# Kernel tuning notes

Measured on AMD Instinct MI355X. Metric: run time of the kernel, lower is better.

## Reference

```python
import jax, jax.numpy as jnp
import numpy as np

BLANK = 0


def setup_inputs() -> dict:
    key = jax.random.key(0)
    k1, k2 = jax.random.split(key)
    B, T, V = 64, 4096, 128
    feature = jax.random.normal(k1, (B, T, V), dtype=jnp.float32)
    lengths = jax.random.randint(k2, (B,), 1, T + 1, dtype=jnp.int32)
    return {"feature": feature, "lengths": lengths, "beam_width": 1}


def reference(feature, lengths, beam_width):
    # Greedy CTC decode (beam_width <= 1 path of the torch module), fully vectorized.
    # feature: (B, T, V) raw logits; lengths: (B,) valid frame counts.
    B, T, V = feature.shape
    logp = jax.nn.log_softmax(feature.astype(jnp.float32), axis=-1)  # (B, T, V)
    max_scores = jnp.max(logp, axis=-1)                               # (B, T)
    tokens = jnp.argmax(logp, axis=-1).astype(jnp.int32)              # (B, T)

    tmask = jnp.arange(T)[None, :] < lengths[:, None]                 # (B, T) valid frames
    logp_scores = jnp.sum(jnp.where(tmask, max_scores, 0.0), axis=-1) # (B,)

    # CTC collapse: keep token iff it is not blank and differs from previous frame's token.
    # (t != prev or prev == blank) and t != blank  ==  (t != blank) and (t != prev)
    prev = jnp.concatenate(
        [jnp.full((B, 1), BLANK, dtype=tokens.dtype), tokens[:, :-1]], axis=1
    )
    keep = (tokens != BLANK) & (tokens != prev) & tmask               # (B, T)

    # Fixed-shape encoding of the ragged prediction lists:
    # tokens[b, t] is part of prediction[b] (in time order) wherever keep[b, t].
    return tokens, keep, logp_scores
```

## Files before the change

kernel.cpp:

```cpp
#include <hip/hip_runtime.h>

#define BLANK 0

__global__ __launch_bounds__(256) void ctc_rowmax(const float* __restrict__ feat,
                                                  float* __restrict__ out_tok,
                                                  float* __restrict__ row_score,
                                                  int BT)
{
    int pair = blockIdx.x * 4 + (threadIdx.x >> 6);
    int lane = threadIdx.x & 63;
    int l32  = lane & 31;
    int row  = pair * 2 + (lane >> 5);
    if (row >= BT) return;

    const float4* p = (const float4*)(feat + (size_t)pair * 256);
    float4 v = p[lane];

    float m = v.x; int idx = l32 * 4;
    if (v.y > m) { m = v.y; idx = l32 * 4 + 1; }
    if (v.z > m) { m = v.z; idx = l32 * 4 + 2; }
    if (v.w > m) { m = v.w; idx = l32 * 4 + 3; }

    #pragma unroll
    for (int off = 16; off >= 1; off >>= 1) {
        float om = __shfl_xor(m, off, 64);
        int   oi = __shfl_xor(idx, off, 64);
        if (om > m || (om == m && oi < idx)) { m = om; idx = oi; }
    }

    float s = __expf(v.x - m) + __expf(v.y - m) + __expf(v.z - m) + __expf(v.w - m);
    #pragma unroll
    for (int off = 16; off >= 1; off >>= 1) s += __shfl_xor(s, off, 64);

    if (l32 == 0) {
        out_tok[row]   = (float)idx;
        row_score[row] = -__logf(s);
    }
}

__global__ __launch_bounds__(256) void ctc_collapse(const int* __restrict__ lengths,
                                                    const float* __restrict__ out_tok,
                                                    float* __restrict__ keepbuf,
                                                    float* __restrict__ scores,
                                                    int T)
{
    int b = blockIdx.y;
    int t = blockIdx.x * 256 + threadIdx.x;
    float contrib = 0.0f;
    if (t < T) {
        int len = lengths[b];
        size_t base = (size_t)b * T;
        int tk   = (int)out_tok[base + t];
        int prev = (t == 0) ? BLANK : (int)out_tok[base + t - 1];
        float sc = keepbuf[base + t];
        bool valid = t < len;
        keepbuf[base + t] = (tk != BLANK && tk != prev && valid) ? 1.0f : 0.0f;
        contrib = valid ? sc : 0.0f;
    }
    #pragma unroll
    for (int off = 32; off >= 1; off >>= 1) contrib += __shfl_xor(contrib, off, 64);
    if ((threadIdx.x & 63) == 0) atomicAdd(&scores[b], contrib);
}

extern "C" void kernel_launch(void* const* d_in, const int* in_sizes, int n_in,
                              void* d_out, int out_size, void* d_ws, size_t ws_size,
                              hipStream_t stream) {
    const float* feat    = (const float*)d_in[0];
    const int*   lengths = (const int*)d_in[1];

    const int V  = 128;
    const int B  = in_sizes[1];
    const int T  = in_sizes[0] / (B * V);
    const int BT = B * T;

    float* out_tok  = (float*)d_out;
    float* keepbuf  = (float*)d_out + (size_t)BT;
    float* scores   = (float*)d_out + (size_t)2 * BT;

    int pairs  = (BT + 1) / 2;
    int blocks = (pairs + 3) / 4;
    ctc_rowmax<<<blocks, 256, 0, stream>>>(feat, out_tok, keepbuf, BT);

    hipMemsetAsync((void*)scores, 0, (size_t)B * sizeof(float), stream);

    dim3 grid2((T + 255) / 256, B);
    ctc_collapse<<<grid2, 256, 0, stream>>>(lengths, out_tok, keepbuf, scores, T);
}
```

Before: 216.7 us.

## Fuse masked score reduction into rowmax with grid-stride loop and per-8-row partials

The rowmax kernel becomes a grid-stride loop over groups of 8 rows per wavefront with four float4 loads in flight. It computes the log-softmax max as m - log(sum exp(x)) without max subtraction, picks the argmax via ballot instead of index shuffles, and applies the length mask in-kernel, writing one partial sum per 8 rows to workspace. The collapse kernel drops the per-row score buffer read, the memset and the atomics, reducing partials in block 0 of each batch row. Risks: unshifted expf can overflow for large logits, and the shift/mask indexing assumes T is a power of two and BT divisible by 8.

```diff
diff --git a/kernel.cpp b/kernel.cpp
--- a/kernel.cpp
+++ b/kernel.cpp
@@ -3,63 +3,90 @@
 #define BLANK 0
 
 __global__ __launch_bounds__(256) void ctc_rowmax(const float* __restrict__ feat,
+                                                  const int* __restrict__ lengths,
                                                   float* __restrict__ out_tok,
-                                                  float* __restrict__ row_score,
-                                                  int BT)
+                                                  float* __restrict__ partial,
+                                                  int npairs, int Tshift, int Tmask)
 {
-    int pair = blockIdx.x * 4 + (threadIdx.x >> 6);
-    int lane = threadIdx.x & 63;
-    int l32  = lane & 31;
-    int row  = pair * 2 + (lane >> 5);
-    if (row >= BT) return;
+    const int lane = threadIdx.x & 63;
+    const int l32  = lane & 31;
+    const int half = lane >> 5;
+    const int wid  = (blockIdx.x * 256 + (int)threadIdx.x) >> 6;
+    const int nw   = (gridDim.x * 256) >> 6;
+    const int nquads = npairs >> 2;
 
-    const float4* p = (const float4*)(feat + (size_t)pair * 256);
-    float4 v = p[lane];
+    for (int q = wid; q < nquads; q += nw) {
+        const int pair0 = q << 2;
+        const float4* base = (const float4*)feat + (size_t)pair0 * 64;
+        float4 v0 = base[lane];
+        float4 v1 = base[64 + lane];
+        float4 v2 = base[128 + lane];
+        float4 v3 = base[192 + lane];
 
-    float m = v.x; int idx = l32 * 4;
-    if (v.y > m) { m = v.y; idx = l32 * 4 + 1; }
-    if (v.z > m) { m = v.z; idx = l32 * 4 + 2; }
-    if (v.w > m) { m = v.w; idx = l32 * 4 + 3; }
+        const int row0 = pair0 << 1;
+        const int len  = lengths[row0 >> Tshift];
+        float acc = 0.0f;
 
-    #pragma unroll
-    for (int off = 16; off >= 1; off >>= 1) {
-        float om = __shfl_xor(m, off, 64);
-        int   oi = __shfl_xor(idx, off, 64);
-        if (om > m || (om == m && oi < idx)) { m = om; idx = oi; }
-    }
+        auto process = [&](float4 v, int pair) {
+            float m = v.x; int li = 0;
+            if (v.y > m) { m = v.y; li = 1; }
+            if (v.z > m) { m = v.z; li = 2; }
+            if (v.w > m) { m = v.w; li = 3; }
+            const float lm  = m;
+            const int  lidx = (l32 << 2) + li;
+            float s = __expf(v.x) + __expf(v.y) + __expf(v.z) + __expf(v.w);
+            #pragma unroll
+            for (int off = 16; off >= 1; off >>= 1) {
+                m  = fmaxf(m, __shfl_xor(m, off, 64));
+                s += __shfl_xor(s, off, 64);
+            }
+            unsigned long long bal = __ballot(lm == m);
+            unsigned seg = half ? (unsigned)(bal >> 32) : (unsigned)bal;
+            int src = (__ffs(seg) - 1) | (half << 5);
+            int idx = __shfl(lidx, src, 64);
+            const int row = (pair << 1) + half;
+            if (l32 == 0) {
+                out_tok[row] = (float)idx;
+                if ((row & Tmask) < len) acc += m - __logf(s);
+            }
+        };
+        process(v0, pair0);
+        process(v1, pair0 + 1);
+        process(v2, pair0 + 2);
+        process(v3, pair0 + 3);
 
-    float s = __expf(v.x - m) + __expf(v.y - m) + __expf(v.z - m) + __expf(v.w - m);
-    #pragma unroll
-    for (int off = 16; off >= 1; off >>= 1) s += __shfl_xor(s, off, 64);
-
-    if (l32 == 0) {
-        out_tok[row]   = (float)idx;
-        row_score[row] = -__logf(s);
+        acc += __shfl_xor(acc, 32, 64);
+        if (lane == 0) partial[row0 >> 3] = acc;
     }
 }
 
 __global__ __launch_bounds__(256) void ctc_collapse(const int* __restrict__ lengths,
                                                     const float* __restrict__ out_tok,
-                                                    float* __restrict__ keepbuf,
+                                                    const float* __restrict__ partial,
+                                                    float* __restrict__ keep,
                                                     float* __restrict__ scores,
-                                                    int T)
+                                                    int T, int Tdiv8)
 {
-    int b = blockIdx.y;
-    int t = blockIdx.x * 256 + threadIdx.x;
-    float contrib = 0.0f;
+    const int b = blockIdx.y;
+    const int t = blockIdx.x * 256 + (int)threadIdx.x;
+    const size_t base = (size_t)b * T;
     if (t < T) {
-        int len = lengths[b];
-        size_t base = (size_t)b * T;
-        int tk   = (int)out_tok[base + t];
-        int prev = (t == 0) ? BLANK : (int)out_tok[base + t - 1];
-        float sc = keepbuf[base + t];
-        bool valid = t < len;
-        keepbuf[base + t] = (tk != BLANK && tk != prev && valid) ? 1.0f : 0.0f;
-        contrib = valid ? sc : 0.0f;
+        float tk = out_tok[base + t];
+        float pv = (t == 0) ? (float)BLANK : out_tok[base + t - 1];
+        bool valid = t < lengths[b];
+        keep[base + t] = (tk != (float)BLANK && tk != pv && valid) ? 1.0f : 0.0f;
     }
-    #pragma unroll
-    for (int off = 32; off >= 1; off >>= 1) contrib += __shfl_xor(contrib, off, 64);
-    if ((threadIdx.x & 63) == 0) atomicAdd(&scores[b], contrib);
+    if (blockIdx.x == 0) {
+        float s = 0.0f;
+        for (int i = threadIdx.x; i < Tdiv8; i += 256)
+            s += partial[(size_t)b * Tdiv8 + i];
+        #pragma unroll
+        for (int off = 32; off >= 1; off >>= 1) s += __shfl_xor(s, off, 64);
+        __shared__ float red[4];
+        if ((threadIdx.x & 63) == 0) red[threadIdx.x >> 6] = s;
+        __syncthreads();
+        if (threadIdx.x == 0) scores[b] = red[0] + red[1] + red[2] + red[3];
+    }
 }
 
 extern "C" void kernel_launch(void* const* d_in, const int* in_sizes, int n_in,
@@ -73,16 +100,19 @@
     const int T  = in_sizes[0] / (B * V);
     const int BT = B * T;
 
-    float* out_tok  = (float*)d_out;
-    float* keepbuf  = (float*)d_out + (size_t)BT;
-    float* scores   = (float*)d_out + (size_t)2 * BT;
+    float* out_tok = (float*)d_out;
+    float* keep    = out_tok + (size_t)BT;
+    float* scores  = out_tok + (size_t)2 * BT;
+    float* partial = (float*)d_ws;
 
-    int pairs  = (BT + 1) / 2;
-    int blocks = (pairs + 3) / 4;
-    ctc_rowmax<<<blocks, 256, 0, stream>>>(feat, out_tok, keepbuf, BT);
+    int Tshift = 31 - __builtin_clz((unsigned)T);
+    int Tmask  = T - 1;
+    int npairs = BT >> 1;
 
-    hipMemsetAsync((void*)scores, 0, (size_t)B * sizeof(float), stream);
+    ctc_rowmax<<<2048, 256, 0, stream>>>(feat, lengths, out_tok, partial,
+                                         npairs, Tshift, Tmask);
 
-    dim3 grid2((T + 255) / 256, B);
-    ctc_collapse<<<grid2, 256, 0, stream>>>(lengths, out_tok, keepbuf, scores, T);
+    dim3 g2((T + 255) / 256, B);
+    ctc_collapse<<<g2, 256, 0, stream>>>(lengths, out_tok, partial, keep, scores,
+                                         T, T >> 3);
 }
```

After: 192.2 us. 1.13x faster.
